# Kernel optimization log

Hardware: AMD Instinct MI355X
Metric: run time of the kernel (lower is better)

## Reference

```python
import jax, jax.numpy as jnp
import numpy as np
from itertools import combinations

NDIM = 256
BATCH = 65536


def setup_inputs() -> dict:
    key = jax.random.key(0)
    k1, k2 = jax.random.split(key)
    pairs = np.array(list(combinations(range(NDIM), 2)), dtype=np.int32)  # [comb(ndim,2), 2]
    return {
        "x": jax.random.normal(k1, (BATCH, NDIM), dtype=jnp.float32),
        "rots": jax.random.normal(k2, (pairs.shape[0],), dtype=jnp.float32),
        "idx_i": jnp.asarray(pairs[:, 0]),
        "idx_j": jnp.asarray(pairs[:, 1]),
    }


def _build_mat(rots, idx_i, idx_j, ndim):
    # Equivalent to mat = R_last @ ... @ R_first @ I, then return mat.T.
    # Each Givens rotation R_(i,j,theta) only mixes rows i and j, so we update
    # two rows per step (O(ndim) work) instead of a dense ndim x ndim matmul.
    # Torch uses cfloat, but all imaginary parts are identically zero, so
    # float32 computes the same math.
    def step(mat, t):
        i, j, theta = t
        c = jnp.cos(theta)
        s = jnp.sin(theta)
        ri = mat[i]
        rj = mat[j]
        mat = mat.at[i].set(c * ri - s * rj)
        mat = mat.at[j].set(s * ri + c * rj)
        return mat, None

    mat0 = jnp.eye(ndim, dtype=rots.dtype)
    mat, _ = jax.lax.scan(step, mat0, (idx_i, idx_j, rots))
    return mat.T  # forward does x @ mat.T


def reference(x, rots, idx_i, idx_j):
    m = _build_mat(rots, idx_i, idx_j, x.shape[-1])  # [ndim, ndim]
    return x @ m
```

## Files before the change

### kernel.cpp

```cpp
#include <hip/hip_runtime.h>
#include <hip/hip_bf16.h>
#include <math.h>

#define NDIM 256
#define NROT 32640
#define NSEG 64
#define MATE (NDIM * NDIM)
#define NODEE (2 * MATE)

#define BF 1280
#define BC 16
#define CSLMAX 1104

typedef __bf16 bf16x4_t __attribute__((ext_vector_type(4)));
typedef __bf16 bf16x8_t __attribute__((ext_vector_type(8)));
typedef float f32x4_t __attribute__((ext_vector_type(4)));


#define ROT1(RJ, CS) { float nri_ = fmaf((CS).x, ri, -((CS).y * (RJ))); \
                       (RJ) = fmaf((CS).y, ri, (CS).x * (RJ)); ri = nri_; }

#define LOAD16(P, JB, KK) \
    P##0 = *(const f32x4_t*)&tile[(JB)][t][0]; \
    P##1 = *(const f32x4_t*)&tile[(JB)][t][4]; \
    P##2 = *(const f32x4_t*)&tile[(JB) + 1][t][0]; \
    P##3 = *(const f32x4_t*)&tile[(JB) + 1][t][4]; \
    _Pragma("unroll") \
    for (int u = 0; u < 16; u++) P##c[u] = csl[(KK) + u];

#define COMP16(P, JB) \
    _Pragma("unroll") \
    for (int u = 0; u < 4; u++) ROT1(P##0[u], P##c[u]) \
    _Pragma("unroll") \
    for (int u = 0; u < 4; u++) ROT1(P##1[u], P##c[4 + u]) \
    _Pragma("unroll") \
    for (int u = 0; u < 4; u++) ROT1(P##2[u], P##c[8 + u]) \
    _Pragma("unroll") \
    for (int u = 0; u < 4; u++) ROT1(P##3[u], P##c[12 + u]) \
    *(f32x4_t*)&tile[(JB)][t][0] = P##0; \
    *(f32x4_t*)&tile[(JB)][t][4] = P##1; \
    *(f32x4_t*)&tile[(JB) + 1][t][0] = P##2; \
    *(f32x4_t*)&tile[(JB) + 1][t][4] = P##3;

__device__ __forceinline__ int run_off(int r) {
    return 255 * r - (r * (r - 1)) / 2;
}
__device__ __forceinline__ int cum_cost(int r) {
    return BF * r + BC * run_off(r);
}
__device__ __forceinline__ int seg_boundary(int s) {
    if (s <= 0) return 0;
    if (s >= NSEG) return 255;
    const long target = ((long)cum_cost(255) * s) / NSEG;
    int lo = 0, hi = 255;
    while (lo < hi) {
        int mid = (lo + hi) >> 1;
        if ((long)cum_cost(mid) >= target) hi = mid; else lo = mid + 1;
    }
    return lo;
}

__global__ __launch_bounds__(64, 1) void k_build(const float* __restrict__ rots,
                                                 __bf16* __restrict__ leaves) {
    __shared__ float tile[32][64][8];
    __shared__ float2 csl[CSLMAX];
    const int t = threadIdx.x;
    const int seg = blockIdx.x >> 2;
    const int cg_ = blockIdx.x & 3;
    const int col = cg_ * 64 + t;

    const int r0 = seg_boundary(seg);
    const int r1 = seg_boundary(seg + 1);
    const int kg0 = run_off(r0);
    const int nrot = run_off(r1) - kg0;

    for (int u = t; u < nrot; u += 64) {
        float th = rots[kg0 + u];
        float s, c;
        sincosf(th, &s, &c);
        csl[u] = make_float2(c, s);
    }
    for (int u = nrot + t; u < nrot + 16 && u < CSLMAX; u += 64) csl[u] = make_float2(1.f, 0.f);

    #pragma unroll
    for (int jb = 0; jb < 32; jb++) {
        f32x4_t z0 = {0.f, 0.f, 0.f, 0.f}, z1 = {0.f, 0.f, 0.f, 0.f};
        if ((col >> 3) == jb) {
            if ((col & 7) < 4) z0[col & 3] = 1.0f;
            else               z1[col & 3] = 1.0f;
        }
        *(f32x4_t*)&tile[jb][t][0] = z0;
        *(f32x4_t*)&tile[jb][t][4] = z1;
    }

    float* T = &tile[0][0][0];
    #define TADDR(r) ((((r) >> 3) * 512) + t * 8 + ((r) & 7))

    int k = 0;
    for (int i = r0; i < r1; ++i) {
        float ri = T[TADDR(i)];
        int j = i + 1;
        int rem = NDIM - j;

        int npeel = min((8 - (j & 7)) & 7, rem);
        for (int u = 0; u < npeel; u++) {
            float2 cs = csl[k];
            float rj = T[TADDR(j)];
            float nri = fmaf(cs.x, ri, -(cs.y * rj));
            T[TADDR(j)] = fmaf(cs.y, ri, cs.x * rj);
            ri = nri; j++; k++;
        }
        rem -= npeel;

        if (rem >= 16) {
            int jb = j >> 3;
            f32x4_t A0, A1, A2, A3, B0, B1, B2, B3;
            float2 Ac[16], Bc[16];
            LOAD16(A, jb, k)
            while (rem >= 48) {
                LOAD16(B, jb + 2, k + 16)
                COMP16(A, jb)
                jb += 2; j += 16; k += 16; rem -= 16;
                LOAD16(A, jb + 2, k + 16)
                COMP16(B, jb)
                jb += 2; j += 16; k += 16; rem -= 16;
            }
            if (rem >= 32) {
                LOAD16(B, jb + 2, k + 16)
                COMP16(A, jb)
                jb += 2; j += 16; k += 16; rem -= 16;
                COMP16(B, jb)
                jb += 2; j += 16; k += 16; rem -= 16;
            } else {
                COMP16(A, jb)
                jb += 2; j += 16; k += 16; rem -= 16;
            }
        }

        if (rem >= 8) {
            int jb = j >> 3;
            f32x4_t a0 = *(const f32x4_t*)&tile[jb][t][0];
            f32x4_t a1 = *(const f32x4_t*)&tile[jb][t][4];
            float2 cc[8];
            #pragma unroll
            for (int u = 0; u < 8; u++) cc[u] = csl[k + u];
            #pragma unroll
            for (int u = 0; u < 4; u++) ROT1(a0[u], cc[u])
            #pragma unroll
            for (int u = 0; u < 4; u++) ROT1(a1[u], cc[4 + u])
            *(f32x4_t*)&tile[jb][t][0] = a0;
            *(f32x4_t*)&tile[jb][t][4] = a1;
            j += 8; k += 8; rem -= 8;
        }

        while (rem > 0) {
            float2 cs = csl[k];
            float rj = T[TADDR(j)];
            float nri = fmaf(cs.x, ri, -(cs.y * rj));
            T[TADDR(j)] = fmaf(cs.y, ri, cs.x * rj);
            ri = nri; j++; k++; rem--;
        }

        T[TADDR(i)] = ri;
    }
    #undef TADDR

    __bf16* hi = leaves + (size_t)seg * NODEE;
    __bf16* lo = hi + MATE;
    if (seg & 1) {
        for (int jb = 0; jb < 32; jb++) {
            f32x4_t v0 = *(const f32x4_t*)&tile[jb][t][0];
            f32x4_t v1 = *(const f32x4_t*)&tile[jb][t][4];
            #pragma unroll
            for (int u = 0; u < 8; u++) {
                float v = (u < 4) ? v0[u & 3] : v1[u & 3];
                __bf16 h = (__bf16)v;
                hi[(size_t)(jb * 8 + u) * NDIM + col] = h;
                lo[(size_t)(jb * 8 + u) * NDIM + col] = (__bf16)(v - (float)h);
            }
        }
    } else {
        for (int jb = 0; jb < 32; jb++) {
            f32x4_t v0 = *(const f32x4_t*)&tile[jb][t][0];
            f32x4_t v1 = *(const f32x4_t*)&tile[jb][t][4];
            bf16x8_t vh, vl;
            #pragma unroll
            for (int u = 0; u < 8; u++) {
                float v = (u < 4) ? v0[u & 3] : v1[u & 3];
                __bf16 h = (__bf16)v;
                vh[u] = h;
                vl[u] = (__bf16)(v - (float)h);
            }
            *(bf16x8_t*)&hi[(size_t)col * NDIM + jb * 8] = vh;
            *(bf16x8_t*)&lo[(size_t)col * NDIM + jb * 8] = vl;
        }
    }
}

#define LDK2 136
__global__ __launch_bounds__(256, 2) void k_combine(const __bf16* __restrict__ src,
                                                    __bf16* __restrict__ dst,
                                                    int finalLevel) {
    __shared__ __bf16 planes[4][64 * LDK2];

    const int p = blockIdx.x >> 4;
    const int qd = blockIdx.x & 15;
    const int rbq = (qd >> 2) * 64;
    const int cbq = (qd & 3) * 64;
    const __bf16* A = src + (size_t)(2 * p) * NODEE;
    const __bf16* B = src + (size_t)(2 * p + 1) * NODEE;
    __bf16* Chi = dst + (size_t)p * NODEE;
    __bf16* Clo = Chi + MATE;
    const bool storeT = (!finalLevel) && ((p & 1) == 0);

    const int t = threadIdx.x;
    const int wid = t >> 6, lane = t & 63;
    const int wr2 = (wid >> 1) * 32, wc2 = (wid & 1) * 32;
    const int lrow = lane & 15, kg = lane >> 4;

    const __bf16* plane_src[4] = {B, B + MATE, A, A + MATE};
    const int plane_row0[4] = {rbq, rbq, cbq, cbq};

    #pragma unroll
    for (int q = 0; q < 16; q++) {
        int g = q * 256 + t;
        int pl = g >> 10;
        int c = g & 1023;
        int row = c >> 4, sg = c & 15;
        bf16x8_t v = *(const bf16x8_t*)&plane_src[pl][(size_t)(plane_row0[pl] + row) * NDIM + sg * 8];
        *(bf16x8_t*)&planes[pl][row * LDK2 + sg * 8] = v;
    }
    __syncthreads();

    bf16x8_t pre[16];
    #pragma unroll
    for (int q = 0; q < 16; q++) {
        int g = q * 256 + t;
        int pl = g >> 10;
        int c = g & 1023;
        int row = c >> 4, sg = c & 15;
        pre[q] = *(const bf16x8_t*)&plane_src[pl][(size_t)(plane_row0[pl] + row) * NDIM + 128 + sg * 8];
    }

    f32x4_t acc[2][2] = {};
    #pragma unroll
    for (int kc = 0; kc < 4; kc++) {
        bf16x8_t afh[2], afl[2], bfh[2], bfl[2];
        #pragma unroll
        for (int mt = 0; mt < 2; mt++) {
            int r = (wr2 + mt * 16 + lrow) * LDK2 + kc * 32 + kg * 8;
            afh[mt] = *(const bf16x8_t*)&planes[0][r];
            afl[mt] = *(const bf16x8_t*)&planes[1][r];
        }
        #pragma unroll
        for (int nt = 0; nt < 2; nt++) {
            int r = (wc2 + nt * 16 + lrow) * LDK2 + kc * 32 + kg * 8;
            bfh[nt] = *(const bf16x8_t*)&planes[2][r];
            bfl[nt] = *(const bf16x8_t*)&planes[3][r];
        }
        #pragma unroll
        for (int mt = 0; mt < 2; mt++)
            #pragma unroll
            for (int nt = 0; nt < 2; nt++) {
                acc[mt][nt] = __builtin_amdgcn_mfma_f32_16x16x32_bf16(afh[mt], bfh[nt], acc[mt][nt], 0, 0, 0);
                acc[mt][nt] = __builtin_amdgcn_mfma_f32_16x16x32_bf16(afh[mt], bfl[nt], acc[mt][nt], 0, 0, 0);
                acc[mt][nt] = __builtin_amdgcn_mfma_f32_16x16x32_bf16(afl[mt], bfh[nt], acc[mt][nt], 0, 0, 0);
            }
    }
    __syncthreads();

    #pragma unroll
    for (int q = 0; q < 16; q++) {
        int g = q * 256 + t;
        int pl = g >> 10;
        int c = g & 1023;
        int row = c >> 4, sg = c & 15;
        *(bf16x8_t*)&planes[pl][row * LDK2 + sg * 8] = pre[q];
    }
    __syncthreads();

    #pragma unroll
    for (int kc = 0; kc < 4; kc++) {
        bf16x8_t afh[2], afl[2], bfh[2], bfl[2];
        #pragma unroll
        for (int mt = 0; mt < 2; mt++) {
            int r = (wr2 + mt * 16 + lrow) * LDK2 + kc * 32 + kg * 8;
            afh[mt] = *(const bf16x8_t*)&planes[0][r];
            afl[mt] = *(const bf16x8_t*)&planes[1][r];
        }
        #pragma unroll
        for (int nt = 0; nt < 2; nt++) {
            int r = (wc2 + nt * 16 + lrow) * LDK2 + kc * 32 + kg * 8;
            bfh[nt] = *(const bf16x8_t*)&planes[2][r];
            bfl[nt] = *(const bf16x8_t*)&planes[3][r];
        }
        #pragma unroll
        for (int mt = 0; mt < 2; mt++)
            #pragma unroll
            for (int nt = 0; nt < 2; nt++) {
                acc[mt][nt] = __builtin_amdgcn_mfma_f32_16x16x32_bf16(afh[mt], bfh[nt], acc[mt][nt], 0, 0, 0);
                acc[mt][nt] = __builtin_amdgcn_mfma_f32_16x16x32_bf16(afh[mt], bfl[nt], acc[mt][nt], 0, 0, 0);
                acc[mt][nt] = __builtin_amdgcn_mfma_f32_16x16x32_bf16(afl[mt], bfh[nt], acc[mt][nt], 0, 0, 0);
            }
    }

    #pragma unroll
    for (int mt = 0; mt < 2; mt++)
        #pragma unroll
        for (int nt = 0; nt < 2; nt++) {
            int grow = rbq + wr2 + mt * 16 + kg * 4;
            int gcol = cbq + wc2 + nt * 16 + lrow;
            if (storeT) {
                bf16x4_t vh, vl;
                #pragma unroll
                for (int r = 0; r < 4; r++) {
                    float v = acc[mt][nt][r];
                    __bf16 h = (__bf16)v;
                    vh[r] = h;
                    vl[r] = (__bf16)(v - (float)h);
                }
                *(bf16x4_t*)&Chi[(size_t)gcol * NDIM + grow] = vh;
                *(bf16x4_t*)&Clo[(size_t)gcol * NDIM + grow] = vl;
            } else if (finalLevel) {
                #pragma unroll
                for (int r = 0; r < 4; r++)
                    Chi[(size_t)(grow + r) * NDIM + gcol] = (__bf16)acc[mt][nt][r];
            } else {
                #pragma unroll
                for (int r = 0; r < 4; r++) {
                    float v = acc[mt][nt][r];
                    __bf16 h = (__bf16)v;
                    Chi[(size_t)(grow + r) * NDIM + gcol] = h;
                    Clo[(size_t)(grow + r) * NDIM + gcol] = (__bf16)(v - (float)h);
                }
            }
        }
}

#define LDA 72
__global__ __launch_bounds__(256, 2) void k_gemm(const float* __restrict__ X,
                                                 const __bf16* __restrict__ Mhi,
                                                 float* __restrict__ Y,
                                                 int rowOff) {
    __shared__ __bf16 As[128 * LDA];
    __shared__ __bf16 Bs[128 * LDA];
    const int bx = blockIdx.x;
    const int xcd = bx & 7;
    const int q = bx >> 3;
    const int bn = (q & 1) * 128;
    const int bm = (xcd + (q >> 1) * 8) * 128 + rowOff;
    const int t = threadIdx.x;
    const int wid = t >> 6;
    const int lane = t & 63;
    const int wr = (wid >> 1) * 64;
    const int wc = (wid & 1) * 64;
    const int lrow = lane & 15;
    const int kg = lane >> 4;

    f32x4_t acc[4][4] = {};

    f32x4_t ra[8];
    bf16x8_t rb[4];

    #pragma unroll
    for (int qq = 0; qq < 8; qq++) {
        int g = qq * 256 + t;
        ra[qq] = *(const f32x4_t*)&X[(size_t)(bm + (g >> 4)) * 256 + (g & 15) * 4];
    }
    #pragma unroll
    for (int qq = 0; qq < 4; qq++) {
        int g = qq * 256 + t;
        rb[qq] = *(const bf16x8_t*)&Mhi[(size_t)(bn + (g >> 3)) * 256 + (g & 7) * 8];
    }

    #pragma unroll
    for (int it = 0; it < 4; it++) {
        #pragma unroll
        for (int qq = 0; qq < 8; qq++) {
            int g = qq * 256 + t;
            f32x4_t v = ra[qq];
            bf16x4_t h = {(__bf16)v.x, (__bf16)v.y, (__bf16)v.z, (__bf16)v.w};
            *(bf16x4_t*)&As[(g >> 4) * LDA + (g & 15) * 4] = h;
        }
        #pragma unroll
        for (int qq = 0; qq < 4; qq++) {
            int g = qq * 256 + t;
            *(bf16x8_t*)&Bs[(g >> 3) * LDA + (g & 7) * 8] = rb[qq];
        }
        __syncthreads();

        if (it < 3) {
            int kc = (it + 1) * 64;
            #pragma unroll
            for (int qq = 0; qq < 8; qq++) {
                int g = qq * 256 + t;
                ra[qq] = *(const f32x4_t*)&X[(size_t)(bm + (g >> 4)) * 256 + kc + (g & 15) * 4];
            }
            #pragma unroll
            for (int qq = 0; qq < 4; qq++) {
                int g = qq * 256 + t;
                rb[qq] = *(const bf16x8_t*)&Mhi[(size_t)(bn + (g >> 3)) * 256 + kc + (g & 7) * 8];
            }
        }

        #pragma unroll
        for (int k2 = 0; k2 < 2; k2++) {
            bf16x8_t af[4], bfr[4];
            #pragma unroll
            for (int mt = 0; mt < 4; mt++)
                af[mt] = *(const bf16x8_t*)&As[(wr + mt * 16 + lrow) * LDA + k2 * 32 + kg * 8];
            #pragma unroll
            for (int nt = 0; nt < 4; nt++)
                bfr[nt] = *(const bf16x8_t*)&Bs[(wc + nt * 16 + lrow) * LDA + k2 * 32 + kg * 8];
            #pragma unroll
            for (int mt = 0; mt < 4; mt++)
                #pragma unroll
                for (int nt = 0; nt < 4; nt++)
                    acc[mt][nt] = __builtin_amdgcn_mfma_f32_16x16x32_bf16(af[mt], bfr[nt], acc[mt][nt], 0, 0, 0);
        }
        __syncthreads();
    }

    const int ocol = bn + wc + lrow;
    const int orow = bm + wr + kg * 4;
    #pragma unroll
    for (int mt = 0; mt < 4; mt++)
        #pragma unroll
        for (int nt = 0; nt < 4; nt++)
            #pragma unroll
            for (int r = 0; r < 4; r++)
                Y[(size_t)(orow + mt * 16 + r) * 256 + ocol + nt * 16] = acc[mt][nt][r];
}

extern "C" void kernel_launch(void* const* d_in, const int* in_sizes, int n_in,
                              void* d_out, int out_size, void* d_ws, size_t ws_size,
                              hipStream_t stream) {
    const float* x = (const float*)d_in[0];
    const float* rots = (const float*)d_in[1];
    float* out = (float*)d_out;

    __bf16* B0 = (__bf16*)d_ws;
    __bf16* B1 = B0 + (size_t)NSEG * NODEE;

    k_build<<<NSEG * 4, 64, 0, stream>>>(rots, B0);
    k_combine<<<32 * 16, 256, 0, stream>>>(B0, B1, 0);
    k_combine<<<16 * 16, 256, 0, stream>>>(B1, B0, 0);
    k_combine<<<8 * 16, 256, 0, stream>>>(B0, B1, 0);
    k_combine<<<4 * 16, 256, 0, stream>>>(B1, B0, 0);
    k_combine<<<2 * 16, 256, 0, stream>>>(B0, B1, 0);
    k_combine<<<1 * 16, 256, 0, stream>>>(B1, B0, 1);
    k_gemm<<<512, 256, 0, stream>>>(x, B0, out, 0);
    k_gemm<<<512, 256, 0, stream>>>(x, B0, out, 32768);
}
```

Measured before the change: 217.9 us.

## Replace binary combine tree with 4-way chained products per column strip

The six pairwise combine launches are replaced by three k_chain launches. Each block owns a 16-column strip of a 4-matrix group and multiplies it through three successive A matrices, keeping the intermediate strip in LDS in split bf16 hi/lo form. The leaf transpose parity changes to match the 4-way grouping, and the two half-batch GEMM launches merge into one launch of 1024 blocks. This cuts launch count and global round-trips for intermediates, but the first chain level has fewer, larger blocks that stream A straight from global memory, and the chained steps inside a block run serially.

```diff
diff --git a/kernel.cpp b/kernel.cpp
--- a/kernel.cpp
+++ b/kernel.cpp
@@ -167,7 +167,7 @@
 
     __bf16* hi = leaves + (size_t)seg * NODEE;
     __bf16* lo = hi + MATE;
-    if (seg & 1) {
+    if (seg & 3) {
         for (int jb = 0; jb < 32; jb++) {
             f32x4_t v0 = *(const f32x4_t*)&tile[jb][t][0];
             f32x4_t v1 = *(const f32x4_t*)&tile[jb][t][4];
@@ -197,158 +197,138 @@
     }
 }
 
-#define LDK2 136
-__global__ __launch_bounds__(256, 2) void k_combine(const __bf16* __restrict__ src,
-                                                    __bf16* __restrict__ dst,
-                                                    int finalLevel) {
-    __shared__ __bf16 planes[4][64 * LDK2];
-
-    const int p = blockIdx.x >> 4;
-    const int qd = blockIdx.x & 15;
-    const int rbq = (qd >> 2) * 64;
-    const int cbq = (qd & 3) * 64;
-    const __bf16* A = src + (size_t)(2 * p) * NODEE;
-    const __bf16* B = src + (size_t)(2 * p + 1) * NODEE;
-    __bf16* Chi = dst + (size_t)p * NODEE;
+#define LDS2 264
+__global__ __launch_bounds__(512, 1) void k_chain(const __bf16* __restrict__ src,
+                                                  __bf16* __restrict__ dst,
+                                                  int finalLevel) {
+    __shared__ __bf16 strip[2][2][16 * LDS2];
+
+    const int node = blockIdx.x >> 4;
+    const int sid = blockIdx.x & 15;
+    const __bf16* c0 = src + (size_t)(4 * node) * NODEE;
+    const __bf16* a1 = src + (size_t)(4 * node + 1) * NODEE;
+    const __bf16* a2 = src + (size_t)(4 * node + 2) * NODEE;
+    const __bf16* a3 = src + (size_t)(4 * node + 3) * NODEE;
+    __bf16* Chi = dst + (size_t)node * NODEE;
     __bf16* Clo = Chi + MATE;
-    const bool storeT = (!finalLevel) && ((p & 1) == 0);
+    const bool storeT = (!finalLevel) && ((node & 3) == 0);
 
     const int t = threadIdx.x;
-    const int wid = t >> 6, lane = t & 63;
-    const int wr2 = (wid >> 1) * 32, wc2 = (wid & 1) * 32;
+    const int w = t >> 6, lane = t & 63;
     const int lrow = lane & 15, kg = lane >> 4;
-
-    const __bf16* plane_src[4] = {B, B + MATE, A, A + MATE};
-    const int plane_row0[4] = {rbq, rbq, cbq, cbq};
-
-    #pragma unroll
-    for (int q = 0; q < 16; q++) {
-        int g = q * 256 + t;
-        int pl = g >> 10;
-        int c = g & 1023;
-        int row = c >> 4, sg = c & 15;
-        bf16x8_t v = *(const bf16x8_t*)&plane_src[pl][(size_t)(plane_row0[pl] + row) * NDIM + sg * 8];
-        *(bf16x8_t*)&planes[pl][row * LDK2 + sg * 8] = v;
+    const int r0 = w * 32;
+
+    #pragma unroll
+    for (int q = 0; q < 2; q++) {
+        int g = q * 512 + t;
+        int pl = g >> 9;
+        int c = g & 511;
+        int col = c >> 5, sg = c & 31;
+        bf16x8_t v = *(const bf16x8_t*)&c0[(size_t)pl * MATE + (size_t)(sid * 16 + col) * NDIM + sg * 8];
+        *(bf16x8_t*)&strip[0][pl][col * LDS2 + sg * 8] = v;
     }
     __syncthreads();
 
-    bf16x8_t pre[16];
-    #pragma unroll
-    for (int q = 0; q < 16; q++) {
-        int g = q * 256 + t;
-        int pl = g >> 10;
-        int c = g & 1023;
-        int row = c >> 4, sg = c & 15;
-        pre[q] = *(const bf16x8_t*)&plane_src[pl][(size_t)(plane_row0[pl] + row) * NDIM + 128 + sg * 8];
-    }
-
-    f32x4_t acc[2][2] = {};
-    #pragma unroll
-    for (int kc = 0; kc < 4; kc++) {
-        bf16x8_t afh[2], afl[2], bfh[2], bfl[2];
+    const __bf16* As[3] = {a1, a2, a3};
+    int cur = 0;
+    #pragma unroll
+    for (int pr = 0; pr < 3; pr++) {
+        const __bf16* Ah = As[pr];
+        const __bf16* Al = Ah + MATE;
+        f32x4_t acc[2] = {};
+        bf16x8_t ah[2], al[2];
         #pragma unroll
         for (int mt = 0; mt < 2; mt++) {
-            int r = (wr2 + mt * 16 + lrow) * LDK2 + kc * 32 + kg * 8;
-            afh[mt] = *(const bf16x8_t*)&planes[0][r];
-            afl[mt] = *(const bf16x8_t*)&planes[1][r];
-        }
-        #pragma unroll
-        for (int nt = 0; nt < 2; nt++) {
-            int r = (wc2 + nt * 16 + lrow) * LDK2 + kc * 32 + kg * 8;
-            bfh[nt] = *(const bf16x8_t*)&planes[2][r];
-            bfl[nt] = *(const bf16x8_t*)&planes[3][r];
-        }
-        #pragma unroll
-        for (int mt = 0; mt < 2; mt++)
-            #pragma unroll
-            for (int nt = 0; nt < 2; nt++) {
-                acc[mt][nt] = __builtin_amdgcn_mfma_f32_16x16x32_bf16(afh[mt], bfh[nt], acc[mt][nt], 0, 0, 0);
-                acc[mt][nt] = __builtin_amdgcn_mfma_f32_16x16x32_bf16(afh[mt], bfl[nt], acc[mt][nt], 0, 0, 0);
-                acc[mt][nt] = __builtin_amdgcn_mfma_f32_16x16x32_bf16(afl[mt], bfh[nt], acc[mt][nt], 0, 0, 0);
-            }
-    }
-    __syncthreads();
-
-    #pragma unroll
-    for (int q = 0; q < 16; q++) {
-        int g = q * 256 + t;
-        int pl = g >> 10;
-        int c = g & 1023;
-        int row = c >> 4, sg = c & 15;
-        *(bf16x8_t*)&planes[pl][row * LDK2 + sg * 8] = pre[q];
-    }
-    __syncthreads();
-
-    #pragma unroll
-    for (int kc = 0; kc < 4; kc++) {
-        bf16x8_t afh[2], afl[2], bfh[2], bfl[2];
-        #pragma unroll
-        for (int mt = 0; mt < 2; mt++) {
-            int r = (wr2 + mt * 16 + lrow) * LDK2 + kc * 32 + kg * 8;
-            afh[mt] = *(const bf16x8_t*)&planes[0][r];
-            afl[mt] = *(const bf16x8_t*)&planes[1][r];
-        }
-        #pragma unroll
-        for (int nt = 0; nt < 2; nt++) {
-            int r = (wc2 + nt * 16 + lrow) * LDK2 + kc * 32 + kg * 8;
-            bfh[nt] = *(const bf16x8_t*)&planes[2][r];
-            bfl[nt] = *(const bf16x8_t*)&planes[3][r];
-        }
-        #pragma unroll
-        for (int mt = 0; mt < 2; mt++)
-            #pragma unroll
-            for (int nt = 0; nt < 2; nt++) {
-                acc[mt][nt] = __builtin_amdgcn_mfma_f32_16x16x32_bf16(afh[mt], bfh[nt], acc[mt][nt], 0, 0, 0);
-                acc[mt][nt] = __builtin_amdgcn_mfma_f32_16x16x32_bf16(afh[mt], bfl[nt], acc[mt][nt], 0, 0, 0);
-                acc[mt][nt] = __builtin_amdgcn_mfma_f32_16x16x32_bf16(afl[mt], bfh[nt], acc[mt][nt], 0, 0, 0);
-            }
-    }
-
-    #pragma unroll
-    for (int mt = 0; mt < 2; mt++)
-        #pragma unroll
-        for (int nt = 0; nt < 2; nt++) {
-            int grow = rbq + wr2 + mt * 16 + kg * 4;
-            int gcol = cbq + wc2 + nt * 16 + lrow;
-            if (storeT) {
+            ah[mt] = *(const bf16x8_t*)&Ah[(size_t)(r0 + mt * 16 + lrow) * NDIM + kg * 8];
+            al[mt] = *(const bf16x8_t*)&Al[(size_t)(r0 + mt * 16 + lrow) * NDIM + kg * 8];
+        }
+        #pragma unroll
+        for (int kc = 0; kc < 8; kc++) {
+            bf16x8_t nh[2], nl[2];
+            if (kc < 7) {
+                #pragma unroll
+                for (int mt = 0; mt < 2; mt++) {
+                    nh[mt] = *(const bf16x8_t*)&Ah[(size_t)(r0 + mt * 16 + lrow) * NDIM + (kc + 1) * 32 + kg * 8];
+                    nl[mt] = *(const bf16x8_t*)&Al[(size_t)(r0 + mt * 16 + lrow) * NDIM + (kc + 1) * 32 + kg * 8];
+                }
+            }
+            bf16x8_t bh = *(const bf16x8_t*)&strip[cur][0][lrow * LDS2 + kc * 32 + kg * 8];
+            bf16x8_t bl = *(const bf16x8_t*)&strip[cur][1][lrow * LDS2 + kc * 32 + kg * 8];
+            #pragma unroll
+            for (int mt = 0; mt < 2; mt++) {
+                acc[mt] = __builtin_amdgcn_mfma_f32_16x16x32_bf16(ah[mt], bh, acc[mt], 0, 0, 0);
+                acc[mt] = __builtin_amdgcn_mfma_f32_16x16x32_bf16(ah[mt], bl, acc[mt], 0, 0, 0);
+                acc[mt] = __builtin_amdgcn_mfma_f32_16x16x32_bf16(al[mt], bh, acc[mt], 0, 0, 0);
+            }
+            if (kc < 7) {
+                #pragma unroll
+                for (int mt = 0; mt < 2; mt++) { ah[mt] = nh[mt]; al[mt] = nl[mt]; }
+            }
+        }
+
+        if (pr < 2) {
+            const int nxt = cur ^ 1;
+            #pragma unroll
+            for (int mt = 0; mt < 2; mt++) {
                 bf16x4_t vh, vl;
                 #pragma unroll
                 for (int r = 0; r < 4; r++) {
-                    float v = acc[mt][nt][r];
+                    float v = acc[mt][r];
                     __bf16 h = (__bf16)v;
                     vh[r] = h;
                     vl[r] = (__bf16)(v - (float)h);
                 }
-                *(bf16x4_t*)&Chi[(size_t)gcol * NDIM + grow] = vh;
-                *(bf16x4_t*)&Clo[(size_t)gcol * NDIM + grow] = vl;
-            } else if (finalLevel) {
-                #pragma unroll
-                for (int r = 0; r < 4; r++)
-                    Chi[(size_t)(grow + r) * NDIM + gcol] = (__bf16)acc[mt][nt][r];
-            } else {
-                #pragma unroll
-                for (int r = 0; r < 4; r++) {
-                    float v = acc[mt][nt][r];
-                    __bf16 h = (__bf16)v;
-                    Chi[(size_t)(grow + r) * NDIM + gcol] = h;
-                    Clo[(size_t)(grow + r) * NDIM + gcol] = (__bf16)(v - (float)h);
+                int kpos = r0 + mt * 16 + kg * 4;
+                *(bf16x4_t*)&strip[nxt][0][lrow * LDS2 + kpos] = vh;
+                *(bf16x4_t*)&strip[nxt][1][lrow * LDS2 + kpos] = vl;
+            }
+            __syncthreads();
+            cur = nxt;
+        } else {
+            const int gcol = sid * 16 + lrow;
+            #pragma unroll
+            for (int mt = 0; mt < 2; mt++) {
+                int grow = r0 + mt * 16 + kg * 4;
+                if (storeT) {
+                    bf16x4_t vh, vl;
+                    #pragma unroll
+                    for (int r = 0; r < 4; r++) {
+                        float v = acc[mt][r];
+                        __bf16 h = (__bf16)v;
+                        vh[r] = h;
+                        vl[r] = (__bf16)(v - (float)h);
+                    }
+                    *(bf16x4_t*)&Chi[(size_t)gcol * NDIM + grow] = vh;
+                    *(bf16x4_t*)&Clo[(size_t)gcol * NDIM + grow] = vl;
+                } else if (finalLevel) {
+                    #pragma unroll
+                    for (int r = 0; r < 4; r++)
+                        Chi[(size_t)(grow + r) * NDIM + gcol] = (__bf16)acc[mt][r];
+                } else {
+                    #pragma unroll
+                    for (int r = 0; r < 4; r++) {
+                        float v = acc[mt][r];
+                        __bf16 h = (__bf16)v;
+                        Chi[(size_t)(grow + r) * NDIM + gcol] = h;
+                        Clo[(size_t)(grow + r) * NDIM + gcol] = (__bf16)(v - (float)h);
+                    }
                 }
             }
         }
+    }
 }
 
 #define LDA 72
 __global__ __launch_bounds__(256, 2) void k_gemm(const float* __restrict__ X,
                                                  const __bf16* __restrict__ Mhi,
-                                                 float* __restrict__ Y,
-                                                 int rowOff) {
+                                                 float* __restrict__ Y) {
     __shared__ __bf16 As[128 * LDA];
     __shared__ __bf16 Bs[128 * LDA];
     const int bx = blockIdx.x;
     const int xcd = bx & 7;
     const int q = bx >> 3;
     const int bn = (q & 1) * 128;
-    const int bm = (xcd + (q >> 1) * 8) * 128 + rowOff;
+    const int bm = (xcd + (q >> 1) * 8) * 128;
     const int t = threadIdx.x;
     const int wid = t >> 6;
     const int lane = t & 63;
@@ -443,12 +423,8 @@
     __bf16* B1 = B0 + (size_t)NSEG * NODEE;
 
     k_build<<<NSEG * 4, 64, 0, stream>>>(rots, B0);
-    k_combine<<<32 * 16, 256, 0, stream>>>(B0, B1, 0);
-    k_combine<<<16 * 16, 256, 0, stream>>>(B1, B0, 0);
-    k_combine<<<8 * 16, 256, 0, stream>>>(B0, B1, 0);
-    k_combine<<<4 * 16, 256, 0, stream>>>(B1, B0, 0);
-    k_combine<<<2 * 16, 256, 0, stream>>>(B0, B1, 0);
-    k_combine<<<1 * 16, 256, 0, stream>>>(B1, B0, 1);
-    k_gemm<<<512, 256, 0, stream>>>(x, B0, out, 0);
-    k_gemm<<<512, 256, 0, stream>>>(x, B0, out, 32768);
-}
+    k_chain<<<16 * 16, 512, 0, stream>>>(B0, B1, 0);
+    k_chain<<<4 * 16, 512, 0, stream>>>(B1, B0, 0);
+    k_chain<<<1 * 16, 512, 0, stream>>>(B0, B1, 1);
+    k_gemm<<<1024, 256, 0, stream>>>(x, B1, out);
+}
```

Result: slower. 233.5 us (+7.1%).
